# Kernel optimization log

Hardware: AMD Instinct MI355X
Metric: run time of the kernel (lower is better)

Reference implementation:

```python
import jax, jax.numpy as jnp
import numpy as np

N = 100000      # number of nodes
D = 64          # node_dim
H = 128         # hidden
E = 1600000     # number of undirected edges (each yields 2 directed messages)


def setup_inputs() -> dict:
    key = jax.random.key(0)
    k_nodes, k_edges, k_w1, k_w2 = jax.random.split(key, 4)
    nodes = jax.random.normal(k_nodes, (N, D), dtype=jnp.float32)
    edges = jax.random.randint(k_edges, (E, 2), 0, N, dtype=jnp.int32)
    # msg = Linear(2D, H) -> ReLU -> Linear(H, D); Kaiming-ish init
    W1 = jax.random.normal(k_w1, (2 * D, H), dtype=jnp.float32) * (1.0 / np.sqrt(2 * D))
    b1 = jnp.zeros((H,), dtype=jnp.float32)
    W2 = jax.random.normal(k_w2, (H, D), dtype=jnp.float32) * (1.0 / np.sqrt(H))
    b2 = jnp.zeros((D,), dtype=jnp.float32)
    return {"nodes": nodes, "edges": edges, "W1": W1, "b1": b1, "W2": W2, "b2": b2}


def reference(nodes, edges, W1, b1, W2, b2):
    # nodes: [N, D]; edges: [E, 2] int32
    i = edges[:, 0]
    j = edges[:, 1]
    h_i = nodes[i]            # [E, D] gather
    h_j = nodes[j]            # [E, D] gather

    def mlp(x):               # [E, 2D] -> [E, D]
        return jax.nn.relu(x @ W1 + b1) @ W2 + b2

    m_ij = mlp(jnp.concatenate([h_i, h_j], axis=-1))  # message to node i
    m_ji = mlp(jnp.concatenate([h_j, h_i], axis=-1))  # message to node j

    # out = nodes.clone(); out[i] += m_ij; out[j] += m_ji  (all from ORIGINAL nodes)
    out = nodes \
        + jax.ops.segment_sum(m_ij, i, num_segments=N) \
        + jax.ops.segment_sum(m_ji, j, num_segments=N)
    return out
```

## Files before the change

### kernel.cpp

```cpp
#include <hip/hip_runtime.h>

#define NEDGES 1600000
#define NNODES 100000
#define OVCAP  (1 << 19)

typedef __bf16 bf16x8 __attribute__((ext_vector_type(8)));
typedef __bf16 bf16x4 __attribute__((ext_vector_type(4)));
typedef float f32x4 __attribute__((ext_vector_type(4)));
typedef unsigned short u16x8 __attribute__((ext_vector_type(8)));

__device__ __forceinline__ __bf16 f2bf(float f) {
  unsigned u = __builtin_bit_cast(unsigned, f);
  u += 0x7FFFu + ((u >> 16) & 1u);
  unsigned short s = (unsigned short)(u >> 16);
  return __builtin_bit_cast(__bf16, s);
}


__device__ __forceinline__ void cvt_row(const float* __restrict__ nodes, int t,
                                        __bf16* __restrict__ nbf) {
  float4 v0 = ((const float4*)nodes)[t * 2];
  float4 v1 = ((const float4*)nodes)[t * 2 + 1];
  bf16x8 o;
  o[0] = f2bf(v0.x); o[1] = f2bf(v0.y); o[2] = f2bf(v0.z); o[3] = f2bf(v0.w);
  o[4] = f2bf(v1.x); o[5] = f2bf(v1.y); o[6] = f2bf(v1.z); o[7] = f2bf(v1.w);
  ((bf16x8*)nbf)[t] = o;
}

__device__ __forceinline__ void weight_img(const float* __restrict__ W1,
                                           const float* __restrict__ W2,
                                           int t, __bf16* __restrict__ wimg) {
  if (t < 16384) {
    int k = t >> 7, n = t & 127;
    wimg[n * 128 + (((k >> 3) ^ (n & 15)) << 3) + (k & 7)] = f2bf(W1[t]);
  } else if (t < 24576) {
    int u = t - 16384;
    int k = u >> 6, n = u & 63;
    wimg[16384 + n * 128 + (((k >> 3) ^ (n & 15)) << 3) + (k & 7)] = f2bf(W2[u]);
  }
}


__global__ void prep_k(const float* __restrict__ nodes,
                       const float* __restrict__ W1,
                       const float* __restrict__ W2,
                       unsigned* __restrict__ cnt,
                       unsigned* __restrict__ ovn,
                       __bf16* __restrict__ wimg,
                       __bf16* __restrict__ nbf) {
  const int t = blockIdx.x * 256 + threadIdx.x;
  cvt_row(nodes, t, nbf);
  weight_img(W1, W2, t, wimg);
  if (t < NNODES) cnt[t] = 0u;
  if (t == 0) *ovn = 0u;
}

__global__ void build_k(const int* __restrict__ edges,
                        unsigned* __restrict__ cnt,
                        unsigned* __restrict__ rec,
                        unsigned* __restrict__ ovf,
                        unsigned* __restrict__ ovn,
                        int cap) {
  const int t = blockIdx.x * 256 + threadIdx.x;
  int2 e = ((const int2*)edges)[t];
  unsigned s0 = atomicAdd(&cnt[e.x], 1u);
  unsigned s1 = atomicAdd(&cnt[e.y], 1u);
  if ((int)s0 < cap) rec[(long)e.x * cap + s0] = (unsigned)e.y;
  else { unsigned p = atomicAdd(ovn, 1u);
         if (p < OVCAP) { ovf[2 * p] = (unsigned)e.x; ovf[2 * p + 1] = (unsigned)e.y; } }
  if ((int)s1 < cap) rec[(long)e.y * cap + s1] = (unsigned)e.x;
  else { unsigned p = atomicAdd(ovn, 1u);
         if (p < OVCAP) { ovf[2 * p] = (unsigned)e.y; ovf[2 * p + 1] = (unsigned)e.x; } }
}

__global__ void ovf_k(const float* __restrict__ nodes,
                      const float* __restrict__ W1, const float* __restrict__ b1,
                      const float* __restrict__ W2, const float* __restrict__ b2,
                      const unsigned* __restrict__ ovf,
                      const unsigned* __restrict__ ovn,
                      float* __restrict__ out) {
  unsigned n = *ovn; if (n > OVCAP) n = OVCAP;
  const unsigned total = n * 64u;
  for (unsigned idx = blockIdx.x * blockDim.x + threadIdx.x; idx < total;
       idx += gridDim.x * blockDim.x) {
    const unsigned r = idx >> 6; const int d = (int)(idx & 63u);
    const int v = (int)ovf[2 * r], u = (int)ovf[2 * r + 1];
    const float* hv = nodes + (long)v * 64;
    const float* hu = nodes + (long)u * 64;
    float md = b2[d];
    for (int h = 0; h < 128; ++h) {
      float s = b1[h];
      for (int k = 0; k < 64; ++k)
        s += hv[k] * W1[k * 128 + h] + hu[k] * W1[(64 + k) * 128 + h];
      s = s > 0.f ? s : 0.f;
      md += s * W2[h * 64 + d];
    }
    atomicAdd(out + (long)v * 64 + d, md);
  }
}

__launch_bounds__(256, 2)
__global__ void gnn_k(const __bf16* __restrict__ nbf,
                      const float* __restrict__ nodes,
                      const unsigned* __restrict__ cntoff,
                      const unsigned* __restrict__ rec,
                      const __bf16* __restrict__ wimg,
                      const float* __restrict__ b1,
                      const float* __restrict__ b2,
                      float* __restrict__ out) {
  __shared__ __align__(16) __bf16 w1t[128 * 128];
  __shared__ __align__(16) __bf16 w2t[64 * 128];
  __shared__ __align__(16) __bf16 hid[4][16 * 128];

  const int tid = threadIdx.x;

  {
    const u16x8* s1 = (const u16x8*)wimg;
    u16x8* d1 = (u16x8*)w1t;
#pragma unroll
    for (int it = 0; it < 8; ++it) d1[it * 256 + tid] = s1[it * 256 + tid];
    const u16x8* s2 = (const u16x8*)(wimg + 16384);
    u16x8* d2 = (u16x8*)w2t;
#pragma unroll
    for (int it = 0; it < 4; ++it) d2[it * 256 + tid] = s2[it * 256 + tid];
  }
  __syncthreads();

  const int lane = tid & 63, wave = tid >> 6;
  const int col = lane & 15, quad = lane >> 4;
  __bf16* myhid = hid[wave];

  const float b2l = b2[lane];

  const int bid = blockIdx.x;
  const int wg = (bid & 7) * 3125 + (bid >> 3);
  const int v = wg * 4 + wave;

  const unsigned c = cntoff[v];
  const int deg = (c < 64u) ? (int)c : 64;
  const long base = (long)v * 64;
  const int ntile = (deg + 15) >> 4;

  int ridx = v;
  if (lane < deg) ridx = (int)rec[base + lane];

  f32x4 accv[8];
  {
    const bf16x8* vrow = (const bf16x8*)(nbf + (long)v * 64);
    const bf16x8 v0f = vrow[quad];
    const bf16x8 v1f = vrow[4 + quad];
#pragma unroll
    for (int nt = 0; nt < 8; ++nt)
      accv[nt] = *(const f32x4*)&b1[nt * 16 + quad * 4];
#pragma unroll
    for (int kt = 0; kt < 2; ++kt) {
      const int kblk = kt * 4 + quad;
      const bf16x8 bx = kt ? v1f : v0f;
#pragma unroll
      for (int nt = 0; nt < 8; ++nt) {
        const int n = nt * 16 + col;
        const bf16x8 aw = *(const bf16x8*)&w1t[n * 128 + ((kblk ^ (n & 15)) << 3)];
        accv[nt] = __builtin_amdgcn_mfma_f32_16x16x32_bf16(aw, bx, accv[nt], 0, 0, 0);
      }
    }
  }

  float part[4] = {0.f, 0.f, 0.f, 0.f};

  bf16x8 a2, a3;
  {
    const int o0n = __shfl(ridx, col, 64);
    const bf16x8* orow = (const bf16x8*)(nbf + (long)o0n * 64);
    a2 = orow[quad]; a3 = orow[4 + quad];
  }

  for (int t = 0; t < ntile; ++t) {
    const int tb = t * 16;

    const int onx = __shfl(ridx, (tb + 16 + col) & 63, 64);
    const bf16x8* prow = (const bf16x8*)(nbf + (long)onx * 64);
    const bf16x8 p2 = prow[quad];
    const bf16x8 p3 = prow[4 + quad];

#pragma unroll
    for (int nt = 0; nt < 8; ++nt) {
      const int n = nt * 16 + col;
      const bf16x8 A2 = *(const bf16x8*)&w1t[n * 128 + (((8 + quad) ^ (n & 15)) << 3)];
      const bf16x8 A3 = *(const bf16x8*)&w1t[n * 128 + (((12 + quad) ^ (n & 15)) << 3)];
      f32x4 h = __builtin_amdgcn_mfma_f32_16x16x32_bf16(A2, a2, accv[nt], 0, 0, 0);
      h = __builtin_amdgcn_mfma_f32_16x16x32_bf16(A3, a3, h, 0, 0, 0);
      bf16x4 hp;
#pragma unroll
      for (int r = 0; r < 4; ++r) {
        float x = h[r];
        hp[r] = f2bf(x > 0.0f ? x : 0.0f);
      }
      const int hblk = nt * 2 + (quad >> 1);
      *(bf16x4*)&myhid[col * 128 + ((hblk ^ col) << 3) + ((quad & 1) << 2)] = hp;
    }

    f32x4 acc2[4];
#pragma unroll
    for (int nt = 0; nt < 4; ++nt) acc2[nt] = (f32x4)0.0f;
#pragma unroll
    for (int kt = 0; kt < 4; ++kt) {
      const int kblk = kt * 4 + quad;
      const bf16x8 ah = *(const bf16x8*)&myhid[col * 128 + ((kblk ^ col) << 3)];
#pragma unroll
      for (int nt = 0; nt < 4; ++nt) {
        const int n = nt * 16 + col;
        const bf16x8 bw = *(const bf16x8*)&w2t[n * 128 + ((kblk ^ (n & 15)) << 3)];
        acc2[nt] = __builtin_amdgcn_mfma_f32_16x16x32_bf16(ah, bw, acc2[nt], 0, 0, 0);
      }
    }

    if (tb + 16 <= deg) {
#pragma unroll
      for (int nt = 0; nt < 4; ++nt)
        part[nt] += (acc2[nt][0] + acc2[nt][1]) + (acc2[nt][2] + acc2[nt][3]);
    } else {
#pragma unroll
      for (int r = 0; r < 4; ++r) {
        const bool valid = (tb + quad * 4 + r) < deg;
#pragma unroll
        for (int nt = 0; nt < 4; ++nt) part[nt] += valid ? acc2[nt][r] : 0.0f;
      }
    }

    a2 = p2; a3 = p3;
  }

#pragma unroll
  for (int nt = 0; nt < 4; ++nt) {
    part[nt] += __shfl_xor(part[nt], 16, 64);
    part[nt] += __shfl_xor(part[nt], 32, 64);
  }
  const float v01 = (quad & 1) ? part[1] : part[0];
  const float v23 = (quad & 1) ? part[3] : part[2];
  const float val = (quad & 2) ? v23 : v01;

  const long o = (long)v * 64 + lane;
  out[o] = nodes[o] + val + (float)deg * b2l;
}

__launch_bounds__(256, 2)
__global__ void gnn_csr_k(const __bf16* __restrict__ nbf,
                          const float* __restrict__ nodes,
                          const unsigned* __restrict__ off,
                          const unsigned* __restrict__ rec,
                          const __bf16* __restrict__ wimg,
                          const float* __restrict__ b1,
                          const float* __restrict__ b2,
                          float* __restrict__ out) {
  __shared__ __align__(16) __bf16 w1t[128 * 128];
  __shared__ __align__(16) __bf16 w2t[64 * 128];
  __shared__ __align__(16) __bf16 hid[4][16 * 128];

  const int tid = threadIdx.x;
  {
    const u16x8* s1 = (const u16x8*)wimg;
    u16x8* d1 = (u16x8*)w1t;
#pragma unroll
    for (int it = 0; it < 8; ++it) d1[it * 256 + tid] = s1[it * 256 + tid];
    const u16x8* s2 = (const u16x8*)(wimg + 16384);
    u16x8* d2 = (u16x8*)w2t;
#pragma unroll
    for (int it = 0; it < 4; ++it) d2[it * 256 + tid] = s2[it * 256 + tid];
  }
  __syncthreads();

  const int lane = tid & 63, wave = tid >> 6;
  const int col = lane & 15, quad = lane >> 4;
  __bf16* myhid = hid[wave];
  const float b2l = b2[lane];

  const int bid = blockIdx.x;
  const int wg = (bid & 7) * 3125 + (bid >> 3);
  const int v = wg * 4 + wave;

  const unsigned o0 = off[v];
  const int deg = (int)(off[v + 1] - o0);
  const long base = (long)o0;
  const int ntile = (deg + 15) >> 4;

  f32x4 accv[8];
  {
    const bf16x8* vrow = (const bf16x8*)(nbf + (long)v * 64);
    const bf16x8 v0f = vrow[quad];
    const bf16x8 v1f = vrow[4 + quad];
#pragma unroll
    for (int nt = 0; nt < 8; ++nt)
      accv[nt] = *(const f32x4*)&b1[nt * 16 + quad * 4];
#pragma unroll
    for (int kt = 0; kt < 2; ++kt) {
      const int kblk = kt * 4 + quad;
      const bf16x8 bx = kt ? v1f : v0f;
#pragma unroll
      for (int nt = 0; nt < 8; ++nt) {
        const int n = nt * 16 + col;
        const bf16x8 aw = *(const bf16x8*)&w1t[n * 128 + ((kblk ^ (n & 15)) << 3)];
        accv[nt] = __builtin_amdgcn_mfma_f32_16x16x32_bf16(aw, bx, accv[nt], 0, 0, 0);
      }
    }
  }

  float part[4] = {0.f, 0.f, 0.f, 0.f};

  bf16x8 a2, a3;
  {
    int o0n = v;
    if (col < deg) o0n = (int)rec[base + col];
    const bf16x8* orow = (const bf16x8*)(nbf + (long)o0n * 64);
    a2 = orow[quad]; a3 = orow[4 + quad];
  }

  for (int t = 0; t < ntile; ++t) {
    const int tb = t * 16;
    int onx = v;
    {
      const int rr = tb + 16 + col;
      if (rr < deg) onx = (int)rec[base + rr];
    }
    const bf16x8* prow = (const bf16x8*)(nbf + (long)onx * 64);
    const bf16x8 p2 = prow[quad];
    const bf16x8 p3 = prow[4 + quad];

#pragma unroll
    for (int nt = 0; nt < 8; ++nt) {
      const int n = nt * 16 + col;
      const bf16x8 A2 = *(const bf16x8*)&w1t[n * 128 + (((8 + quad) ^ (n & 15)) << 3)];
      const bf16x8 A3 = *(const bf16x8*)&w1t[n * 128 + (((12 + quad) ^ (n & 15)) << 3)];
      f32x4 h = __builtin_amdgcn_mfma_f32_16x16x32_bf16(A2, a2, accv[nt], 0, 0, 0);
      h = __builtin_amdgcn_mfma_f32_16x16x32_bf16(A3, a3, h, 0, 0, 0);
      bf16x4 hp;
#pragma unroll
      for (int r = 0; r < 4; ++r) {
        float x = h[r];
        hp[r] = f2bf(x > 0.0f ? x : 0.0f);
      }
      const int hblk = nt * 2 + (quad >> 1);
      *(bf16x4*)&myhid[col * 128 + ((hblk ^ col) << 3) + ((quad & 1) << 2)] = hp;
    }

    f32x4 acc2[4];
#pragma unroll
    for (int nt = 0; nt < 4; ++nt) acc2[nt] = (f32x4)0.0f;
#pragma unroll
    for (int kt = 0; kt < 4; ++kt) {
      const int kblk = kt * 4 + quad;
      const bf16x8 ah = *(const bf16x8*)&myhid[col * 128 + ((kblk ^ col) << 3)];
#pragma unroll
      for (int nt = 0; nt < 4; ++nt) {
        const int n = nt * 16 + col;
        const bf16x8 bw = *(const bf16x8*)&w2t[n * 128 + ((kblk ^ (n & 15)) << 3)];
        acc2[nt] = __builtin_amdgcn_mfma_f32_16x16x32_bf16(ah, bw, acc2[nt], 0, 0, 0);
      }
    }

    if (tb + 16 <= deg) {
#pragma unroll
      for (int nt = 0; nt < 4; ++nt)
        part[nt] += (acc2[nt][0] + acc2[nt][1]) + (acc2[nt][2] + acc2[nt][3]);
    } else {
#pragma unroll
      for (int r = 0; r < 4; ++r) {
        const bool valid = (tb + quad * 4 + r) < deg;
#pragma unroll
        for (int nt = 0; nt < 4; ++nt) part[nt] += valid ? acc2[nt][r] : 0.0f;
      }
    }

    a2 = p2; a3 = p3;
  }

#pragma unroll
  for (int nt = 0; nt < 4; ++nt) {
    part[nt] += __shfl_xor(part[nt], 16, 64);
    part[nt] += __shfl_xor(part[nt], 32, 64);
  }
  const float v01 = (quad & 1) ? part[1] : part[0];
  const float v23 = (quad & 1) ? part[3] : part[2];
  const float val = (quad & 2) ? v23 : v01;

  const long o = (long)v * 64 + lane;
  out[o] = nodes[o] + val + (float)deg * b2l;
}


__global__ void hist_k(const int* __restrict__ edges, unsigned* __restrict__ cnt) {
  const int t = blockIdx.x * 256 + threadIdx.x;
  int4 e = ((const int4*)edges)[t];
  atomicAdd(&cnt[e.x], 1u); atomicAdd(&cnt[e.y], 1u);
  atomicAdd(&cnt[e.z], 1u); atomicAdd(&cnt[e.w], 1u);
}

__global__ void scanA_k(const unsigned* __restrict__ cnt, unsigned* __restrict__ bsum) {
  __shared__ unsigned s[1024];
  const int tid = threadIdx.x;
  const int g = blockIdx.x * 1024 + tid;
  s[tid] = (g < NNODES) ? cnt[g] : 0u;
  __syncthreads();
  for (int d = 512; d > 0; d >>= 1) {
    if (tid < d) s[tid] += s[tid + d];
    __syncthreads();
  }
  if (tid == 0) bsum[blockIdx.x] = s[0];
}

__global__ void scanB_k(const unsigned* __restrict__ cnt,
                        const unsigned* __restrict__ bsum,
                        unsigned* __restrict__ off, unsigned* __restrict__ cur) {
  __shared__ unsigned s[1024];
  const int tid = threadIdx.x;
  const int b = blockIdx.x;
  const int g = b * 1024 + tid;
  unsigned pfx = 0;
  for (int j = 0; j < b; ++j) pfx += bsum[j];
  const unsigned x = (g < NNODES) ? cnt[g] : 0u;
  s[tid] = x;
  __syncthreads();
  for (int d = 1; d < 1024; d <<= 1) {
    unsigned tv = (tid >= d) ? s[tid - d] : 0u;
    __syncthreads();
    s[tid] += tv;
    __syncthreads();
  }
  const unsigned excl = pfx + s[tid] - x;
  if (g < NNODES) { off[g] = excl; cur[g] = excl; }
  if (g == NNODES - 1) off[NNODES] = excl + x;
}

__global__ void scat_k(const int* __restrict__ edges,
                       unsigned* __restrict__ cur, unsigned* __restrict__ rec) {
  const int t = blockIdx.x * 256 + threadIdx.x;
  int4 e = ((const int4*)edges)[t];
#pragma unroll
  for (int h = 0; h < 2; ++h) {
    const int a = h ? e.z : e.x;
    const int b = h ? e.w : e.y;
    rec[atomicAdd(&cur[a], 1u)] = (unsigned)b;
    rec[atomicAdd(&cur[b], 1u)] = (unsigned)a;
  }
}


__global__ void init_out(const float* __restrict__ nodes, float* __restrict__ out) {
  int i = blockIdx.x * blockDim.x + threadIdx.x;
  ((float4*)out)[i] = ((const float4*)nodes)[i];
}

__launch_bounds__(256, 2)
__global__ void edge_mlp(const float* __restrict__ nodes,
                         const int* __restrict__ edges,
                         const float* __restrict__ W1,
                         const float* __restrict__ b1,
                         const float* __restrict__ W2,
                         const float* __restrict__ b2,
                         float* __restrict__ out) {
  __shared__ __bf16 w1t[128 * 128];
  __shared__ __bf16 w2t[64 * 128];
  __shared__ __bf16 hid[4][16 * 128];

  const int tid = threadIdx.x;

  for (int it = 0; it < 16; ++it) {
    int q = it * 256 + tid;
    int k = q >> 5;
    int nc = (q & 31) << 2;
    float4 v = ((const float4*)W1)[q];
    float vv[4] = {v.x, v.y, v.z, v.w};
#pragma unroll
    for (int c = 0; c < 4; ++c) {
      int n = nc + c;
      int blk = (k >> 3) ^ (n & 15);
      w1t[n * 128 + blk * 8 + (k & 7)] = f2bf(vv[c]);
    }
  }
  for (int it = 0; it < 8; ++it) {
    int q = it * 256 + tid;
    int k = q >> 4;
    int nc = (q & 15) << 2;
    float4 v = ((const float4*)W2)[q];
    float vv[4] = {v.x, v.y, v.z, v.w};
#pragma unroll
    for (int c = 0; c < 4; ++c) {
      int n = nc + c;
      int blk = (k >> 3) ^ (n & 15);
      w2t[n * 128 + blk * 8 + (k & 7)] = f2bf(vv[c]);
    }
  }
  __syncthreads();

  const int lane = tid & 63;
  const int wave = tid >> 6;
  const int col = lane & 15;
  const int quad = lane >> 4;
  __bf16* myhid = hid[wave];

  float b1v[8], b2v[4];
#pragma unroll
  for (int nt = 0; nt < 8; ++nt) b1v[nt] = b1[nt * 16 + col];
#pragma unroll
  for (int nt = 0; nt < 4; ++nt) b2v[nt] = b2[nt * 16 + col];

  for (int t = 0; t < 8; ++t) {
    const int e0 = blockIdx.x * 512 + wave * 128 + t * 16;
    const int e = e0 + col;
    const int ie = edges[2 * e];
    const int je = edges[2 * e + 1];

    bf16x8 af[4];
#pragma unroll
    for (int kt = 0; kt < 4; ++kt) {
      int k = kt * 32 + quad * 8;
      const float* src = (k < 64) ? (nodes + (long)ie * 64 + k)
                                  : (nodes + (long)je * 64 + (k - 64));
      float4 v0 = ((const float4*)src)[0];
      float4 v1 = ((const float4*)src)[1];
      bf16x8 a;
      a[0] = f2bf(v0.x); a[1] = f2bf(v0.y); a[2] = f2bf(v0.z); a[3] = f2bf(v0.w);
      a[4] = f2bf(v1.x); a[5] = f2bf(v1.y); a[6] = f2bf(v1.z); a[7] = f2bf(v1.w);
      af[kt] = a;
    }

#pragma unroll
    for (int dir = 0; dir < 2; ++dir) {
      f32x4 acc[8];
#pragma unroll
      for (int nt = 0; nt < 8; ++nt) acc[nt] = (f32x4)0.0f;
#pragma unroll
      for (int kt = 0; kt < 4; ++kt) {
        int kblk = kt * 4 + quad;
        if (dir) kblk ^= 8;
#pragma unroll
        for (int nt = 0; nt < 8; ++nt) {
          int n = nt * 16 + col;
          const bf16x8 bf = *(const bf16x8*)&w1t[n * 128 + ((kblk ^ (n & 15)) << 3)];
          acc[nt] = __builtin_amdgcn_mfma_f32_16x16x32_bf16(af[kt], bf, acc[nt], 0, 0, 0);
        }
      }
#pragma unroll
      for (int nt = 0; nt < 8; ++nt) {
        int unit = nt * 16 + col;
#pragma unroll
        for (int r = 0; r < 4; ++r) {
          int m = quad * 4 + r;
          float h = acc[nt][r] + b1v[nt];
          h = h > 0.0f ? h : 0.0f;
          myhid[m * 128 + (((unit >> 3) ^ m) << 3) + (unit & 7)] = f2bf(h);
        }
      }

      f32x4 acc2[4];
#pragma unroll
      for (int nt = 0; nt < 4; ++nt) acc2[nt] = (f32x4)0.0f;
#pragma unroll
      for (int kt = 0; kt < 4; ++kt) {
        int kblk = kt * 4 + quad;
        const bf16x8 ah = *(const bf16x8*)&myhid[col * 128 + ((kblk ^ col) << 3)];
#pragma unroll
        for (int nt = 0; nt < 4; ++nt) {
          int n = nt * 16 + col;
          const bf16x8 bf = *(const bf16x8*)&w2t[n * 128 + ((kblk ^ (n & 15)) << 3)];
          acc2[nt] = __builtin_amdgcn_mfma_f32_16x16x32_bf16(ah, bf, acc2[nt], 0, 0, 0);
        }
      }

#pragma unroll
      for (int r = 0; r < 4; ++r) {
        int em = quad * 4 + r;
        int node = __shfl(dir == 0 ? ie : je, em, 64);
        float* dst = out + (long)node * 64;
#pragma unroll
        for (int nt = 0; nt < 4; ++nt) {
          atomicAdd(dst + nt * 16 + col, acc2[nt][r] + b2v[nt]);
        }
      }
    }
  }
}


extern "C" void kernel_launch(void* const* d_in, const int* in_sizes, int n_in,
                              void* d_out, int out_size, void* d_ws, size_t ws_size,
                              hipStream_t stream) {
  const float* nodes = (const float*)d_in[0];
  const int*   edges = (const int*)d_in[1];
  const float* W1    = (const float*)d_in[2];
  const float* b1    = (const float*)d_in[3];
  const float* W2    = (const float*)d_in[4];
  const float* b2    = (const float*)d_in[5];
  float* out = (float*)d_out;

  char* w = (char*)d_ws;
  auto al = [](size_t x) { return (x + 255) & ~(size_t)255; };

  const int CAP = 64;

  size_t o = 0;
  unsigned* cnt = (unsigned*)(w + o); o = al(o + (size_t)NNODES * 4);
  unsigned* ovn = (unsigned*)(w + o); o = al(o + 256);
  __bf16* wimg  = (__bf16*)(w + o);   o = al(o + (size_t)24576 * 2);
  __bf16* nbf   = (__bf16*)(w + o);   o = al(o + (size_t)NNODES * 64 * 2);
  unsigned* ovf = (unsigned*)(w + o); o = al(o + (size_t)OVCAP * 2 * 4);
  unsigned* rec2 = (unsigned*)(w + o);
  const size_t need_bucket = o + (size_t)NNODES * CAP * 4;

  size_t c = (size_t)((char*)ovf - w);
  unsigned* off  = (unsigned*)(w + c); c = al(c + ((size_t)NNODES + 1) * 4);
  unsigned* cur  = (unsigned*)(w + c); c = al(c + (size_t)NNODES * 4);
  unsigned* bsum = (unsigned*)(w + c); c = al(c + 128 * 4);
  unsigned* rec  = (unsigned*)(w + c);
  const size_t need_csr = c + (size_t)2 * NEDGES * 4;

  if (d_ws && ws_size >= need_bucket) {
    prep_k<<<3125, 256, 0, stream>>>(nodes, W1, W2, cnt, ovn, wimg, nbf);
    build_k<<<6250, 256, 0, stream>>>(edges, cnt, rec2, ovf, ovn, CAP);
    gnn_k<<<25000, 256, 0, stream>>>(nbf, nodes, cnt, rec2, wimg, b1, b2, out);
    ovf_k<<<104, 256, 0, stream>>>(nodes, W1, b1, W2, b2, ovf, ovn, out);
  } else if (d_ws && ws_size >= need_csr) {
    prep_k<<<3125, 256, 0, stream>>>(nodes, W1, W2, cnt, ovn, wimg, nbf);
    hist_k<<<1563, 256, 0, stream>>>(edges, cnt);
    scanA_k<<<98, 1024, 0, stream>>>(cnt, bsum);
    scanB_k<<<98, 1024, 0, stream>>>(cnt, bsum, off, cur);
    scat_k<<<1563, 256, 0, stream>>>(edges, cur, rec);
    gnn_csr_k<<<25000, 256, 0, stream>>>(nbf, nodes, off, rec, wimg, b1, b2, out);
  } else {
    init_out<<<6250, 256, 0, stream>>>(nodes, out);
    edge_mlp<<<3125, 256, 0, stream>>>(nodes, edges, W1, b1, W2, b2, out);
  }
}
```

Baseline: 648.4 us.

## Build per-node edge buckets via two-pass coarse partition and LDS bucketing

Replaces the single-pass per-node bucket build, which does scattered global atomics and scattered 4-byte stores across a 25.6 MB array, with two passes. First, edges are binned into 800 coarse partitions of 125 nodes using packed 64-bit records. Then one block per partition buckets its edges in shared memory and writes the per-node records and counts out contiguously. This trades random global writes and contended atomics for an extra pass over 3.2M packed records and more workspace. Partition or per-node overflow goes to the existing overflow path.

```diff
diff --git a/kernel.cpp b/kernel.cpp
--- a/kernel.cpp
+++ b/kernel.cpp
@@ -3,11 +3,15 @@
 #define NEDGES 1600000
 #define NNODES 100000
 #define OVCAP  (1 << 19)
+#define NPART  800
+#define NPN    125
+#define PARTCAP 5120
 
 typedef __bf16 bf16x8 __attribute__((ext_vector_type(8)));
 typedef __bf16 bf16x4 __attribute__((ext_vector_type(4)));
 typedef float f32x4 __attribute__((ext_vector_type(4)));
 typedef unsigned short u16x8 __attribute__((ext_vector_type(8)));
+typedef unsigned long long u64;
 
 __device__ __forceinline__ __bf16 f2bf(float f) {
   unsigned u = __builtin_bit_cast(unsigned, f);
@@ -40,11 +44,11 @@
   }
 }
 
-
 __global__ void prep_k(const float* __restrict__ nodes,
                        const float* __restrict__ W1,
                        const float* __restrict__ W2,
                        unsigned* __restrict__ cnt,
+                       unsigned* __restrict__ pcnt,
                        unsigned* __restrict__ ovn,
                        __bf16* __restrict__ wimg,
                        __bf16* __restrict__ nbf) {
@@ -52,7 +56,71 @@
   cvt_row(nodes, t, nbf);
   weight_img(W1, W2, t, wimg);
   if (t < NNODES) cnt[t] = 0u;
+  if (t < NPART) pcnt[t] = 0u;
   if (t == 0) *ovn = 0u;
+}
+
+
+__global__ void part_k(const int* __restrict__ edges,
+                       unsigned* __restrict__ pcnt,
+                       u64* __restrict__ part,
+                       unsigned* __restrict__ ovf,
+                       unsigned* __restrict__ ovn) {
+  const int t = blockIdx.x * 256 + threadIdx.x;
+  int4 e = ((const int4*)edges)[t];
+  const unsigned a0 = (unsigned)e.x, b0 = (unsigned)e.y;
+  const unsigned a1 = (unsigned)e.z, b1 = (unsigned)e.w;
+  const unsigned p0 = a0 / NPN, p1 = b0 / NPN, p2 = a1 / NPN, p3 = b1 / NPN;
+  unsigned s0 = atomicAdd(&pcnt[p0], 1u);
+  unsigned s1 = atomicAdd(&pcnt[p1], 1u);
+  unsigned s2 = atomicAdd(&pcnt[p2], 1u);
+  unsigned s3 = atomicAdd(&pcnt[p3], 1u);
+  if (s0 < PARTCAP) part[(long)p0 * PARTCAP + s0] = ((u64)b0 << 32) | a0;
+  else { unsigned q = atomicAdd(ovn, 1u);
+         if (q < OVCAP) { ovf[2 * q] = a0; ovf[2 * q + 1] = b0; } }
+  if (s1 < PARTCAP) part[(long)p1 * PARTCAP + s1] = ((u64)a0 << 32) | b0;
+  else { unsigned q = atomicAdd(ovn, 1u);
+         if (q < OVCAP) { ovf[2 * q] = b0; ovf[2 * q + 1] = a0; } }
+  if (s2 < PARTCAP) part[(long)p2 * PARTCAP + s2] = ((u64)b1 << 32) | a1;
+  else { unsigned q = atomicAdd(ovn, 1u);
+         if (q < OVCAP) { ovf[2 * q] = a1; ovf[2 * q + 1] = b1; } }
+  if (s3 < PARTCAP) part[(long)p3 * PARTCAP + s3] = ((u64)a1 << 32) | b1;
+  else { unsigned q = atomicAdd(ovn, 1u);
+         if (q < OVCAP) { ovf[2 * q] = b1; ovf[2 * q + 1] = a1; } }
+}
+
+__launch_bounds__(256)
+__global__ void bucket_k(const u64* __restrict__ part,
+                         const unsigned* __restrict__ pcnt,
+                         unsigned* __restrict__ cnt,
+                         unsigned* __restrict__ rec,
+                         unsigned* __restrict__ ovf,
+                         unsigned* __restrict__ ovn) {
+  __shared__ unsigned lcnt[NPN];
+  __shared__ unsigned lrec[NPN * 64];
+  const int tid = threadIdx.x;
+  const int p = blockIdx.x;
+  const int n0 = p * NPN;
+
+  for (int i = tid; i < NPN; i += 256) lcnt[i] = 0u;
+  __syncthreads();
+
+  unsigned m = pcnt[p]; if (m > PARTCAP) m = PARTCAP;
+  for (unsigned r = tid; r < m; r += 256) {
+    const u64 pk = part[(long)p * PARTCAP + r];
+    const unsigned a = (unsigned)pk;
+    const unsigned b = (unsigned)(pk >> 32);
+    const unsigned l = a - (unsigned)n0;
+    const unsigned s = atomicAdd(&lcnt[l], 1u);
+    if (s < 64u) lrec[l * 64 + s] = b;
+    else { unsigned q = atomicAdd(ovn, 1u);
+           if (q < OVCAP) { ovf[2 * q] = a; ovf[2 * q + 1] = b; } }
+  }
+  __syncthreads();
+
+  unsigned* dst = rec + (long)n0 * 64;
+  for (int i = tid; i < NPN * 64; i += 256) dst[i] = lrec[i];
+  for (int i = tid; i < NPN; i += 256) cnt[n0 + i] = lcnt[i];
 }
 
 __global__ void build_k(const int* __restrict__ edges,
@@ -598,28 +666,37 @@
   const int CAP = 64;
 
   size_t o = 0;
-  unsigned* cnt = (unsigned*)(w + o); o = al(o + (size_t)NNODES * 4);
-  unsigned* ovn = (unsigned*)(w + o); o = al(o + 256);
-  __bf16* wimg  = (__bf16*)(w + o);   o = al(o + (size_t)24576 * 2);
-  __bf16* nbf   = (__bf16*)(w + o);   o = al(o + (size_t)NNODES * 64 * 2);
-  unsigned* ovf = (unsigned*)(w + o); o = al(o + (size_t)OVCAP * 2 * 4);
-  unsigned* rec2 = (unsigned*)(w + o);
-  const size_t need_bucket = o + (size_t)NNODES * CAP * 4;
-
-  size_t c = (size_t)((char*)ovf - w);
+  unsigned* cnt  = (unsigned*)(w + o); o = al(o + (size_t)NNODES * 4);
+  unsigned* ovn  = (unsigned*)(w + o); o = al(o + 256);
+  unsigned* pcnt = (unsigned*)(w + o); o = al(o + (size_t)NPART * 4);
+  __bf16* wimg   = (__bf16*)(w + o);   o = al(o + (size_t)24576 * 2);
+  __bf16* nbf    = (__bf16*)(w + o);   o = al(o + (size_t)NNODES * 64 * 2);
+  unsigned* ovf  = (unsigned*)(w + o); o = al(o + (size_t)OVCAP * 2 * 4);
+  unsigned* rec2 = (unsigned*)(w + o); o = al(o + (size_t)NNODES * CAP * 4);
+  const size_t need_bucket = o;
+  u64* part      = (u64*)(w + o);
+  const size_t need_part = o + (size_t)NPART * PARTCAP * 8;
+
+  size_t c = (size_t)((char*)rec2 - w);
   unsigned* off  = (unsigned*)(w + c); c = al(c + ((size_t)NNODES + 1) * 4);
   unsigned* cur  = (unsigned*)(w + c); c = al(c + (size_t)NNODES * 4);
   unsigned* bsum = (unsigned*)(w + c); c = al(c + 128 * 4);
   unsigned* rec  = (unsigned*)(w + c);
   const size_t need_csr = c + (size_t)2 * NEDGES * 4;
 
-  if (d_ws && ws_size >= need_bucket) {
-    prep_k<<<3125, 256, 0, stream>>>(nodes, W1, W2, cnt, ovn, wimg, nbf);
+  if (d_ws && ws_size >= need_part) {
+    prep_k<<<3125, 256, 0, stream>>>(nodes, W1, W2, cnt, pcnt, ovn, wimg, nbf);
+    part_k<<<3125, 256, 0, stream>>>(edges, pcnt, part, ovf, ovn);
+    bucket_k<<<NPART, 256, 0, stream>>>(part, pcnt, cnt, rec2, ovf, ovn);
+    gnn_k<<<25000, 256, 0, stream>>>(nbf, nodes, cnt, rec2, wimg, b1, b2, out);
+    ovf_k<<<104, 256, 0, stream>>>(nodes, W1, b1, W2, b2, ovf, ovn, out);
+  } else if (d_ws && ws_size >= need_bucket) {
+    prep_k<<<3125, 256, 0, stream>>>(nodes, W1, W2, cnt, pcnt, ovn, wimg, nbf);
     build_k<<<6250, 256, 0, stream>>>(edges, cnt, rec2, ovf, ovn, CAP);
     gnn_k<<<25000, 256, 0, stream>>>(nbf, nodes, cnt, rec2, wimg, b1, b2, out);
     ovf_k<<<104, 256, 0, stream>>>(nodes, W1, b1, W2, b2, ovf, ovn, out);
   } else if (d_ws && ws_size >= need_csr) {
-    prep_k<<<3125, 256, 0, stream>>>(nodes, W1, W2, cnt, ovn, wimg, nbf);
+    prep_k<<<3125, 256, 0, stream>>>(nodes, W1, W2, cnt, pcnt, ovn, wimg, nbf);
     hist_k<<<1563, 256, 0, stream>>>(edges, cnt);
     scanA_k<<<98, 1024, 0, stream>>>(cnt, bsum);
     scanB_k<<<98, 1024, 0, stream>>>(cnt, bsum, off, cur);
```

After: 1.120 ms. +72.8%, slower.
